# Kernel optimization log

Hardware: AMD Instinct MI355X
Metric: run time of the kernel (lower is better)

## Reference

```python
import jax, jax.numpy as jnp
import numpy as np

N_NODES = 100000
N_EDGES = 1600000
N_GRAPHS = 512
F_IN = 20
HID = 128
OUT = HID // 2


def _glorot(key, shape):
    fan_in, fan_out = shape[0], shape[1]
    lim = float(np.sqrt(6.0 / (fan_in + fan_out)))
    return jax.random.uniform(key, shape, jnp.float32, -lim, lim)


def setup_inputs() -> dict:
    key = jax.random.key(0)
    ks = jax.random.split(key, 12)
    x = jax.random.normal(ks[0], (N_NODES, F_IN), jnp.float32)
    edge_index = jax.random.randint(ks[1], (2, N_EDGES), 0, N_NODES, dtype=jnp.int64)
    batch = jnp.sort(jax.random.randint(ks[2], (N_NODES,), 0, N_GRAPHS, dtype=jnp.int64))
    return {
        "x": x,
        "edge_index": edge_index,
        "batch": batch,
        "W1": _glorot(ks[3], (F_IN, HID)), "b1": jnp.zeros((HID,), jnp.float32),
        "W2": _glorot(ks[4], (HID, HID)), "b2": jnp.zeros((HID,), jnp.float32),
        "W3": _glorot(ks[5], (HID, HID)), "b3": jnp.zeros((HID,), jnp.float32),
        "Wout": _glorot(ks[6], (HID, OUT)), "bout": jnp.zeros((OUT,), jnp.float32),
    }


def _gcn_conv(x, W, b, src, dst, num_nodes):
    # PyG GCNConv: x' = D^{-1/2} (A + I) D^{-1/2} X W + b (self-loops already in src/dst)
    xw = x @ W                                                  # [N, H]
    ones = jnp.ones(src.shape[0], dtype=xw.dtype)
    deg = jax.ops.segment_sum(ones, dst, num_segments=num_nodes)
    dinv = jnp.where(deg > 0, jax.lax.rsqrt(deg), 0.0)          # [N]
    norm = dinv[src] * dinv[dst]                                # [E+N]
    msg = xw[src] * norm[:, None]                               # gather + scale
    return jax.ops.segment_sum(msg, dst, num_segments=num_nodes) + b


def reference(x, edge_index, batch, W1, b1, W2, b2, W3, b3, Wout, bout):
    num_nodes = x.shape[0]
    loops = jnp.arange(num_nodes, dtype=edge_index.dtype)
    src = jnp.concatenate([edge_index[0], loops])
    dst = jnp.concatenate([edge_index[1], loops])

    h = jax.nn.relu(_gcn_conv(x, W1, b1, src, dst, num_nodes))
    h = jax.nn.relu(_gcn_conv(h, W2, b2, src, dst, num_nodes))
    h = jax.nn.relu(_gcn_conv(h, W3, b3, src, dst, num_nodes))

    # global_mean_pool over graph ids
    sums = jax.ops.segment_sum(h, batch, num_segments=N_GRAPHS)
    counts = jax.ops.segment_sum(jnp.ones(num_nodes, h.dtype), batch, num_segments=N_GRAPHS)
    pooled = sums / jnp.maximum(counts, 1.0)[:, None]           # [G, H]
    return pooled @ Wout + bout                                 # [G, H//2]
```

## Files before the change

kernel.cpp:

```cpp
#include <hip/hip_runtime.h>
#include <hip/hip_fp16.h>

#define N_NODES 100000
#define N_EDGES 1600000
#define N_GRAPHS 512
#define F_IN 20
#define HID 128
#define OUT_F 64

#define BUCKETS 256
#define SPAN 391
#define BCAP 7000
#define EPB 4096

typedef _Float16 half8_t __attribute__((ext_vector_type(8)));
typedef float f32x4_t __attribute__((ext_vector_type(4)));

__device__ inline float4 h4_to_f4(uint2 u) {
    __half2 h0 = *(__half2*)&u.x;
    __half2 h1 = *(__half2*)&u.y;
    float2 f0 = __half22float2(h0);
    float2 f1 = __half22float2(h1);
    return make_float4(f0.x, f0.y, f1.x, f1.y);
}

__global__ __launch_bounds__(512) void partition(const int* __restrict__ src,
                                                 const int* __restrict__ dst,
                                                 int* __restrict__ bpairs,
                                                 int* cur256) {
    __shared__ int lcnt[8][BUCKETS];
    __shared__ int woff[8][BUCKETS];
    int t = threadIdx.x;
    int wv = t >> 6;
    for (int i = t; i < 8 * BUCKETS; i += 512) ((int*)lcnt)[i] = 0;
    __syncthreads();
    int base = blockIdx.x * EPB;
    int myb[8], myp[8], myr[8];
#pragma unroll
    for (int i = 0; i < 8; ++i) {
        int e = base + i * 512 + t;
        int b = -1, p = 0, rk = 0;
        if (e < N_EDGES) {
            int s = src[e], d = dst[e];
            b = d / SPAN;
            p = (s << 9) | (d - b * SPAN);
            rk = atomicAdd(&lcnt[wv][b], 1);
        }
        myb[i] = b; myp[i] = p; myr[i] = rk;
    }
    __syncthreads();
    if (t < BUCKETS) {
        int c[8], tot = 0;
#pragma unroll
        for (int w = 0; w < 8; ++w) { c[w] = lcnt[w][t]; tot += c[w]; }
        int gb = atomicAdd(&cur256[t], tot);
#pragma unroll
        for (int w = 0; w < 8; ++w) { woff[w][t] = gb; gb += c[w]; }
    }
    __syncthreads();
#pragma unroll
    for (int i = 0; i < 8; ++i) {
        int b = myb[i];
        if (b >= 0) {
            int p = woff[wv][b] + myr[i];
            if (p < BCAP) bpairs[(size_t)b * BCAP + p] = myp[i];
        }
    }
}

__global__ __launch_bounds__(512) void csr_build(const int* __restrict__ bpairs,
                                                 const int* __restrict__ cur256,
                                                 int* __restrict__ row_st,
                                                 int* __restrict__ csr,
                                                 const float* __restrict__ x,
                                                 __half* __restrict__ Xs) {
    __shared__ int ocnt[SPAN];
    __shared__ int sc[512];
    __shared__ int cur[SPAN];
    __shared__ int sbase;
    int b = blockIdx.x, t = threadIdx.x;

    int myc = (t < BUCKETS) ? cur256[t] : 0;
    sc[t] = myc;
    __syncthreads();
    for (int o = 1; o < BUCKETS; o <<= 1) {
        int v = (t >= o) ? sc[t - o] : 0;
        __syncthreads();
        sc[t] += v;
        __syncthreads();
    }
    if (t == b) sbase = sc[t] - myc;
    if (b == BUCKETS - 1 && t == 0) row_st[N_NODES] = N_EDGES;

    int n0 = b * SPAN;
    int span = N_NODES - n0; if (span > SPAN) span = SPAN;
    if (t < SPAN) ocnt[t] = 0;
    __syncthreads();

    int n = cur256[b];
    const int* p = bpairs + (size_t)b * BCAP;
    for (int i = t; i < n; i += 512) atomicAdd(&ocnt[p[i] & 511], 1);
    __syncthreads();
    sc[t] = (t < span) ? ocnt[t] : 0;
    __syncthreads();
    for (int o = 1; o < 512; o <<= 1) {
        int v = (t >= o) ? sc[t - o] : 0;
        __syncthreads();
        sc[t] += v;
        __syncthreads();
    }
    int base = sbase;
    if (t < span) {
        int start = sc[t] - ocnt[t];
        row_st[n0 + t] = base + start;
        cur[t] = start;
    }
    __syncthreads();
    for (int i = t; i < n; i += 512) {
        int e = p[i];
        int lp = atomicAdd(&cur[e & 511], 1);
        csr[base + lp] = e >> 9;
    }
    for (int i = t; i < span * 32; i += 512) {
        int nl = i >> 5, f = i & 31;
        float v = (f < F_IN) ? x[(size_t)(n0 + nl) * F_IN + f] : 0.f;
        float di = rsqrtf((float)(ocnt[nl] + 1));
        Xs[(size_t)(n0 + nl) * 32 + f] = __float2half(di * v);
    }
}

__global__ __launch_bounds__(256) void layer1(const __half* __restrict__ Xs,
                                              const int* __restrict__ row_st,
                                              const int* __restrict__ csr,
                                              const float* __restrict__ W,
                                              const float* __restrict__ bias,
                                              __half* __restrict__ H) {
    __shared__ float Wlds[F_IN * HID];
    __shared__ float Alds[16 * F_IN];
    const int t = threadIdx.x;
    const int node0 = blockIdx.x * 16;

    for (int i = t; i < F_IN * HID; i += 256) Wlds[i] = W[i];

    const int h16 = t >> 4;
    const int l16 = t & 15;
    const __half2* X2 = (const __half2*)Xs;
    {
        int nn = node0 + h16;
        int r0 = row_st[nn], r1 = row_st[nn + 1];
        float2 f = __half22float2(X2[(size_t)nn * 16 + l16]);
        float2 acc = f;
        int r = r0;
        for (; r + 1 < r1; r += 2) {
            float2 f0 = __half22float2(X2[(size_t)csr[r] * 16 + l16]);
            float2 f1 = __half22float2(X2[(size_t)csr[r + 1] * 16 + l16]);
            acc.x += f0.x + f1.x;
            acc.y += f0.y + f1.y;
        }
        if (r < r1) {
            float2 f2 = __half22float2(X2[(size_t)csr[r] * 16 + l16]);
            acc.x += f2.x; acc.y += f2.y;
        }
        if (l16 < 10) {
            float di = rsqrtf((float)(r1 - r0 + 1));
            Alds[h16 * F_IN + l16 * 2]     = di * acc.x;
            Alds[h16 * F_IN + l16 * 2 + 1] = di * acc.y;
        }
    }
    __syncthreads();

    const int g  = t >> 5;
    const int h4 = (t & 31) * 4;
    float4 b4 = *(const float4*)&bias[h4];
    float4 acc0 = b4;
    float4 acc1 = b4;
#pragma unroll
    for (int kk = 0; kk < F_IN; ++kk) {
        float a0 = Alds[(g * 2) * F_IN + kk];
        float a1 = Alds[(g * 2 + 1) * F_IN + kk];
        float4 w = *(const float4*)&Wlds[kk * HID + h4];
        acc0.x = fmaf(a0, w.x, acc0.x);
        acc0.y = fmaf(a0, w.y, acc0.y);
        acc0.z = fmaf(a0, w.z, acc0.z);
        acc0.w = fmaf(a0, w.w, acc0.w);
        acc1.x = fmaf(a1, w.x, acc1.x);
        acc1.y = fmaf(a1, w.y, acc1.y);
        acc1.z = fmaf(a1, w.z, acc1.z);
        acc1.w = fmaf(a1, w.w, acc1.w);
    }
    {
        __half2 h0 = __floats2half2_rn(acc0.x, acc0.y);
        __half2 h1 = __floats2half2_rn(acc0.z, acc0.w);
        uint2 u; u.x = *(unsigned*)&h0; u.y = *(unsigned*)&h1;
        ((uint2*)H)[(node0 + g * 2) * 32 + (h4 >> 2)] = u;
    }
    {
        __half2 h0 = __floats2half2_rn(acc1.x, acc1.y);
        __half2 h1 = __floats2half2_rn(acc1.z, acc1.w);
        uint2 u; u.x = *(unsigned*)&h0; u.y = *(unsigned*)&h1;
        ((uint2*)H)[(node0 + g * 2 + 1) * 32 + (h4 >> 2)] = u;
    }
}

__global__ __launch_bounds__(256) void gemm_mfma(const __half* __restrict__ H,
                                                 const float* __restrict__ W,
                                                 const int* __restrict__ row_st,
                                                 __half* __restrict__ T) {
    __shared__ _Float16 Whi[64 * 128];
    __shared__ _Float16 Wlo[64 * 128];
    const int t = threadIdx.x;
    const int c0 = (blockIdx.x & 1) * 64;

    for (int i = t; i < 128 * 64; i += 256) {
        int k = i >> 6, c = i & 63;
        float w = W[k * HID + c0 + c];
        _Float16 hi = (_Float16)w;
        _Float16 lo = (_Float16)((w - (float)hi) * 2048.0f);
        int addr = c * 128 + (((k >> 3) ^ (c & 15)) << 3) + (k & 7);
        Whi[addr] = hi;
        Wlo[addr] = lo;
    }
    __syncthreads();

    const int wv = t >> 6;
    const int l  = t & 63;
    const int lr = l & 15;
    const int lq = l >> 4;

    for (int rep = 0; rep < 4; ++rep) {
        int strip = ((blockIdx.x >> 1) * 4 + wv) * 4 + rep;
        if (strip >= N_NODES / 16) continue;
        int n0 = strip * 16;

        f32x4_t acc[4], acl[4];
#pragma unroll
        for (int ct = 0; ct < 4; ++ct) { acc[ct] = (f32x4_t){0,0,0,0}; acl[ct] = (f32x4_t){0,0,0,0}; }

#pragma unroll
        for (int kc = 0; kc < 4; ++kc) {
            half8_t a = *(const half8_t*)(H + (size_t)(n0 + lr) * 128 + kc * 32 + lq * 8);
#pragma unroll
            for (int j = 0; j < 8; ++j) a[j] = a[j] > (_Float16)0 ? a[j] : (_Float16)0;
            int g = kc * 4 + lq;
#pragma unroll
            for (int ct = 0; ct < 4; ++ct) {
                int c = ct * 16 + lr;
                int addr = c * 128 + ((g ^ lr) << 3);
                half8_t bh = *(const half8_t*)&Whi[addr];
                half8_t bl = *(const half8_t*)&Wlo[addr];
                acc[ct] = __builtin_amdgcn_mfma_f32_16x16x32_f16(a, bh, acc[ct], 0, 0, 0);
                acl[ct] = __builtin_amdgcn_mfma_f32_16x16x32_f16(a, bl, acl[ct], 0, 0, 0);
            }
        }

        int r0 = n0 + lq * 4;
#pragma unroll
        for (int r = 0; r < 4; ++r) {
            int row = r0 + r;
            float d = rsqrtf((float)(row_st[row + 1] - row_st[row] + 1));
#pragma unroll
            for (int ct = 0; ct < 4; ++ct) {
                float v = (acc[ct][r] + acl[ct][r] * 4.8828125e-4f) * d;
                T[(size_t)row * 128 + c0 + ct * 16 + lr] = __float2half(v);
            }
        }
    }
}

__global__ __launch_bounds__(256) void gather_range(const __half* __restrict__ A,
                                                    const int* __restrict__ row_st,
                                                    const int* __restrict__ csr,
                                                    const float* __restrict__ bias,
                                                    __half* __restrict__ B) {
    int t = threadIdx.x;
    int n = blockIdx.x * 8 + (t >> 5);
    int l = t & 31;
    int r0 = row_st[n], r1 = row_st[n + 1];
    float di = rsqrtf((float)(r1 - r0 + 1));
    const uint2* Af = (const uint2*)A;
    float4 acc = h4_to_f4(Af[n * 32 + l]);
    int r = r0;
    for (; r + 7 < r1; r += 8) {
        int s0 = csr[r],     s1 = csr[r + 1], s2 = csr[r + 2], s3 = csr[r + 3];
        int s4 = csr[r + 4], s5 = csr[r + 5], s6 = csr[r + 6], s7 = csr[r + 7];
        float4 v0 = h4_to_f4(Af[s0 * 32 + l]);
        float4 v1 = h4_to_f4(Af[s1 * 32 + l]);
        float4 v2 = h4_to_f4(Af[s2 * 32 + l]);
        float4 v3 = h4_to_f4(Af[s3 * 32 + l]);
        float4 v4 = h4_to_f4(Af[s4 * 32 + l]);
        float4 v5 = h4_to_f4(Af[s5 * 32 + l]);
        float4 v6 = h4_to_f4(Af[s6 * 32 + l]);
        float4 v7 = h4_to_f4(Af[s7 * 32 + l]);
        acc.x += ((v0.x + v1.x) + (v2.x + v3.x)) + ((v4.x + v5.x) + (v6.x + v7.x));
        acc.y += ((v0.y + v1.y) + (v2.y + v3.y)) + ((v4.y + v5.y) + (v6.y + v7.y));
        acc.z += ((v0.z + v1.z) + (v2.z + v3.z)) + ((v4.z + v5.z) + (v6.z + v7.z));
        acc.w += ((v0.w + v1.w) + (v2.w + v3.w)) + ((v4.w + v5.w) + (v6.w + v7.w));
    }
    for (; r + 3 < r1; r += 4) {
        int s0 = csr[r], s1 = csr[r + 1], s2 = csr[r + 2], s3 = csr[r + 3];
        float4 v0 = h4_to_f4(Af[s0 * 32 + l]);
        float4 v1 = h4_to_f4(Af[s1 * 32 + l]);
        float4 v2 = h4_to_f4(Af[s2 * 32 + l]);
        float4 v3 = h4_to_f4(Af[s3 * 32 + l]);
        acc.x += (v0.x + v1.x) + (v2.x + v3.x);
        acc.y += (v0.y + v1.y) + (v2.y + v3.y);
        acc.z += (v0.z + v1.z) + (v2.z + v3.z);
        acc.w += (v0.w + v1.w) + (v2.w + v3.w);
    }
    for (; r < r1; ++r) {
        float4 v = h4_to_f4(Af[csr[r] * 32 + l]);
        acc.x += v.x; acc.y += v.y; acc.z += v.z; acc.w += v.w;
    }
    float4 b4 = ((const float4*)bias)[l];
    __half2 h0 = __floats2half2_rn(fmaf(di, acc.x, b4.x), fmaf(di, acc.y, b4.y));
    __half2 h1 = __floats2half2_rn(fmaf(di, acc.z, b4.z), fmaf(di, acc.w, b4.w));
    uint2 u; u.x = *(unsigned*)&h0; u.y = *(unsigned*)&h1;
    ((uint2*)B)[n * 32 + l] = u;
}

__global__ __launch_bounds__(256) void pool(const __half* __restrict__ B,
                                            const int* __restrict__ batch,
                                            float* sums, float* counts) {
    int t = threadIdx.x;
    int grp = blockIdx.x * 8 + (t >> 5);
    int l = t & 31;
    int h4 = l * 4;
    int n0 = grp * 8;
    if (n0 >= N_NODES) return;
    const uint2* Bf = (const uint2*)B;
    int cur = batch[n0];
    int runlen = 0;
    float4 acc = make_float4(0.f, 0.f, 0.f, 0.f);
    for (int k = 0; k < 8; ++k) {
        int n = n0 + k;
        if (n >= N_NODES) break;
        int g = batch[n];
        if (g != cur) {
            float* sp = &sums[cur * HID + h4];
            atomicAdd(sp + 0, acc.x); atomicAdd(sp + 1, acc.y);
            atomicAdd(sp + 2, acc.z); atomicAdd(sp + 3, acc.w);
            if (l == 0) atomicAdd(&counts[cur], (float)runlen);
            acc = make_float4(0.f, 0.f, 0.f, 0.f);
            runlen = 0;
            cur = g;
        }
        float4 v = h4_to_f4(Bf[n * 32 + l]);
        acc.x += fmaxf(v.x, 0.f);
        acc.y += fmaxf(v.y, 0.f);
        acc.z += fmaxf(v.z, 0.f);
        acc.w += fmaxf(v.w, 0.f);
        ++runlen;
    }
    float* sp = &sums[cur * HID + h4];
    atomicAdd(sp + 0, acc.x); atomicAdd(sp + 1, acc.y);
    atomicAdd(sp + 2, acc.z); atomicAdd(sp + 3, acc.w);
    if (l == 0) atomicAdd(&counts[cur], (float)runlen);
}

__global__ void final_gemm(const float* __restrict__ sums, const float* __restrict__ counts,
                           const float* __restrict__ Wout, const float* __restrict__ bout,
                           float* __restrict__ out) {
    int g = blockIdx.x;
    int o = threadIdx.x;
    __shared__ float p[HID];
    for (int k = o; k < HID; k += 64) p[k] = sums[g * HID + k];
    __syncthreads();
    float inv = 1.0f / fmaxf(counts[g], 1.0f);
    float acc = 0.f;
#pragma unroll 8
    for (int k = 0; k < HID; ++k)
        acc = fmaf(p[k], Wout[k * OUT_F + o], acc);
    out[g * OUT_F + o] = fmaf(inv, acc, bout[o]);
}

extern "C" void kernel_launch(void* const* d_in, const int* in_sizes, int n_in,
                              void* d_out, int out_size, void* d_ws, size_t ws_size,
                              hipStream_t stream) {
    const float* x     = (const float*)d_in[0];
    const int*   ei    = (const int*)d_in[1];
    const int*   batch = (const int*)d_in[2];
    const float* W1    = (const float*)d_in[3];
    const float* b1    = (const float*)d_in[4];
    const float* W2    = (const float*)d_in[5];
    const float* b2    = (const float*)d_in[6];
    const float* W3    = (const float*)d_in[7];
    const float* b3    = (const float*)d_in[8];
    const float* Wout  = (const float*)d_in[9];
    const float* bout  = (const float*)d_in[10];
    float* out = (float*)d_out;

    const int* src = ei;
    const int* dst = ei + N_EDGES;

    float* A      = (float*)d_ws;
    float* Breg   = A + (size_t)N_NODES * HID;
    int*   row_st = (int*)(Breg + (size_t)N_NODES * HID);
    float* sums   = (float*)(row_st + N_NODES + 1);
    float* counts = sums + N_GRAPHS * HID;
    int*   cur256 = (int*)(counts + N_GRAPHS);
    int*   csr    = cur256 + BUCKETS;

    int*    bpairs = (int*)A;
    __half* Xs     = (__half*)((char*)A + 7168000);
    __half* T      = (__half*)A;
    __half* H      = (__half*)Breg;

    hipMemsetAsync(sums, 0, (size_t)(N_GRAPHS * HID + N_GRAPHS + BUCKETS) * 4, stream);
    partition<<<(N_EDGES + EPB - 1) / EPB, 512, 0, stream>>>(src, dst, bpairs, cur256);
    csr_build<<<BUCKETS, 512, 0, stream>>>(bpairs, cur256, row_st, csr, x, Xs);

    layer1<<<N_NODES / 16, 256, 0, stream>>>(Xs, row_st, csr, W1, b1, H);

    gemm_mfma<<<782, 256, 0, stream>>>(H, W2, row_st, T);
    gather_range<<<N_NODES / 8, 256, 0, stream>>>(T, row_st, csr, b2, H);
    gemm_mfma<<<782, 256, 0, stream>>>(H, W3, row_st, T);
    gather_range<<<N_NODES / 8, 256, 0, stream>>>(T, row_st, csr, b3, H);

    pool<<<(N_NODES / 8 + 7) / 8, 256, 0, stream>>>(H, batch, sums, counts);
    final_gemm<<<N_GRAPHS, 64, 0, stream>>>(sums, counts, Wout, bout, out);
}
```

Measured before the change: 386.1 us.

## Fuse mean-pool with output GEMM per graph and double CSR partition buckets

Replaces the atomic-based pooling kernel and separate final GEMM with one kernel per graph that binary-searches the sorted batch array for its node range, reduces in shared memory, and applies Wout. This drops atomics, a kernel launch, and most of the memset. It also doubles the bucket count for CSR construction so each csr_build block handles a smaller span with more parallelism. The per-bucket capacity becomes tight relative to the average bucket load, and overflow is clamped rather than handled.

```diff
diff --git a/kernel.cpp b/kernel.cpp
--- a/kernel.cpp
+++ b/kernel.cpp
@@ -8,9 +8,9 @@
 #define HID 128
 #define OUT_F 64
 
-#define BUCKETS 256
-#define SPAN 391
-#define BCAP 7000
+#define BUCKETS 512
+#define SPAN 196
+#define BCAP 3500
 #define EPB 4096
 
 typedef _Float16 half8_t __attribute__((ext_vector_type(8)));
@@ -27,7 +27,7 @@
 __global__ __launch_bounds__(512) void partition(const int* __restrict__ src,
                                                  const int* __restrict__ dst,
                                                  int* __restrict__ bpairs,
-                                                 int* cur256) {
+                                                 int* cur512) {
     __shared__ int lcnt[8][BUCKETS];
     __shared__ int woff[8][BUCKETS];
     int t = threadIdx.x;
@@ -49,11 +49,11 @@
         myb[i] = b; myp[i] = p; myr[i] = rk;
     }
     __syncthreads();
-    if (t < BUCKETS) {
+    {
         int c[8], tot = 0;
 #pragma unroll
         for (int w = 0; w < 8; ++w) { c[w] = lcnt[w][t]; tot += c[w]; }
-        int gb = atomicAdd(&cur256[t], tot);
+        int gb = atomicAdd(&cur512[t], tot);
 #pragma unroll
         for (int w = 0; w < 8; ++w) { woff[w][t] = gb; gb += c[w]; }
     }
@@ -69,7 +69,7 @@
 }
 
 __global__ __launch_bounds__(512) void csr_build(const int* __restrict__ bpairs,
-                                                 const int* __restrict__ cur256,
+                                                 const int* __restrict__ cur512,
                                                  int* __restrict__ row_st,
                                                  int* __restrict__ csr,
                                                  const float* __restrict__ x,
@@ -80,7 +80,7 @@
     __shared__ int sbase;
     int b = blockIdx.x, t = threadIdx.x;
 
-    int myc = (t < BUCKETS) ? cur256[t] : 0;
+    int myc = cur512[t];
     sc[t] = myc;
     __syncthreads();
     for (int o = 1; o < BUCKETS; o <<= 1) {
@@ -94,10 +94,12 @@
 
     int n0 = b * SPAN;
     int span = N_NODES - n0; if (span > SPAN) span = SPAN;
+    if (span < 0) span = 0;
     if (t < SPAN) ocnt[t] = 0;
     __syncthreads();
 
-    int n = cur256[b];
+    int n = cur512[b];
+    if (n > BCAP) n = BCAP;
     const int* p = bpairs + (size_t)b * BCAP;
     for (int i = t; i < n; i += 512) atomicAdd(&ocnt[p[i] & 511], 1);
     __syncthreads();
@@ -318,59 +320,60 @@
     ((uint2*)B)[n * 32 + l] = u;
 }
 
-__global__ __launch_bounds__(256) void pool(const __half* __restrict__ B,
-                                            const int* __restrict__ batch,
-                                            float* sums, float* counts) {
+__global__ __launch_bounds__(256) void pool_head(const __half* __restrict__ H,
+                                                 const int* __restrict__ batch,
+                                                 const float* __restrict__ Wout,
+                                                 const float* __restrict__ bout,
+                                                 float* __restrict__ out) {
+    __shared__ float4 part[8][32];
+    __shared__ float p[HID];
+    __shared__ int bounds[2];
+    int g = blockIdx.x;
     int t = threadIdx.x;
-    int grp = blockIdx.x * 8 + (t >> 5);
-    int l = t & 31;
-    int h4 = l * 4;
-    int n0 = grp * 8;
-    if (n0 >= N_NODES) return;
-    const uint2* Bf = (const uint2*)B;
-    int cur = batch[n0];
-    int runlen = 0;
+    if (t < 2) {
+        int target = g + t;
+        int lo = 0, hi = N_NODES;
+        while (lo < hi) {
+            int mid = (lo + hi) >> 1;
+            if (batch[mid] < target) lo = mid + 1; else hi = mid;
+        }
+        bounds[t] = lo;
+    }
+    __syncthreads();
+    int lo = bounds[0], hi = bounds[1];
+    int grp = t >> 5, l = t & 31;
+    const uint2* Hf = (const uint2*)H;
     float4 acc = make_float4(0.f, 0.f, 0.f, 0.f);
-    for (int k = 0; k < 8; ++k) {
-        int n = n0 + k;
-        if (n >= N_NODES) break;
-        int g = batch[n];
-        if (g != cur) {
-            float* sp = &sums[cur * HID + h4];
-            atomicAdd(sp + 0, acc.x); atomicAdd(sp + 1, acc.y);
-            atomicAdd(sp + 2, acc.z); atomicAdd(sp + 3, acc.w);
-            if (l == 0) atomicAdd(&counts[cur], (float)runlen);
-            acc = make_float4(0.f, 0.f, 0.f, 0.f);
-            runlen = 0;
-            cur = g;
-        }
-        float4 v = h4_to_f4(Bf[n * 32 + l]);
+    for (int n = lo + grp; n < hi; n += 8) {
+        float4 v = h4_to_f4(Hf[(size_t)n * 32 + l]);
         acc.x += fmaxf(v.x, 0.f);
         acc.y += fmaxf(v.y, 0.f);
         acc.z += fmaxf(v.z, 0.f);
         acc.w += fmaxf(v.w, 0.f);
-        ++runlen;
-    }
-    float* sp = &sums[cur * HID + h4];
-    atomicAdd(sp + 0, acc.x); atomicAdd(sp + 1, acc.y);
-    atomicAdd(sp + 2, acc.z); atomicAdd(sp + 3, acc.w);
-    if (l == 0) atomicAdd(&counts[cur], (float)runlen);
-}
-
-__global__ void final_gemm(const float* __restrict__ sums, const float* __restrict__ counts,
-                           const float* __restrict__ Wout, const float* __restrict__ bout,
-                           float* __restrict__ out) {
-    int g = blockIdx.x;
-    int o = threadIdx.x;
-    __shared__ float p[HID];
-    for (int k = o; k < HID; k += 64) p[k] = sums[g * HID + k];
-    __syncthreads();
-    float inv = 1.0f / fmaxf(counts[g], 1.0f);
-    float acc = 0.f;
+    }
+    part[grp][l] = acc;
+    __syncthreads();
+    if (t < 32) {
+        float4 s = part[0][t];
+#pragma unroll
+        for (int j = 1; j < 8; ++j) {
+            float4 v = part[j][t];
+            s.x += v.x; s.y += v.y; s.z += v.z; s.w += v.w;
+        }
+        float inv = 1.0f / fmaxf((float)(hi - lo), 1.0f);
+        p[t * 4 + 0] = s.x * inv;
+        p[t * 4 + 1] = s.y * inv;
+        p[t * 4 + 2] = s.z * inv;
+        p[t * 4 + 3] = s.w * inv;
+    }
+    __syncthreads();
+    if (t < OUT_F) {
+        float acc2 = 0.f;
 #pragma unroll 8
-    for (int k = 0; k < HID; ++k)
-        acc = fmaf(p[k], Wout[k * OUT_F + o], acc);
-    out[g * OUT_F + o] = fmaf(inv, acc, bout[o]);
+        for (int k = 0; k < HID; ++k)
+            acc2 = fmaf(p[k], Wout[k * OUT_F + t], acc2);
+        out[g * OUT_F + t] = acc2 + bout[t];
+    }
 }
 
 extern "C" void kernel_launch(void* const* d_in, const int* in_sizes, int n_in,
@@ -395,19 +398,17 @@
     float* A      = (float*)d_ws;
     float* Breg   = A + (size_t)N_NODES * HID;
     int*   row_st = (int*)(Breg + (size_t)N_NODES * HID);
-    float* sums   = (float*)(row_st + N_NODES + 1);
-    float* counts = sums + N_GRAPHS * HID;
-    int*   cur256 = (int*)(counts + N_GRAPHS);
-    int*   csr    = cur256 + BUCKETS;
+    int*   cur512 = row_st + N_NODES + 1;
+    int*   csr    = cur512 + BUCKETS;
 
     int*    bpairs = (int*)A;
     __half* Xs     = (__half*)((char*)A + 7168000);
     __half* T      = (__half*)A;
     __half* H      = (__half*)Breg;
 
-    hipMemsetAsync(sums, 0, (size_t)(N_GRAPHS * HID + N_GRAPHS + BUCKETS) * 4, stream);
-    partition<<<(N_EDGES + EPB - 1) / EPB, 512, 0, stream>>>(src, dst, bpairs, cur256);
-    csr_build<<<BUCKETS, 512, 0, stream>>>(bpairs, cur256, row_st, csr, x, Xs);
+    hipMemsetAsync(cur512, 0, BUCKETS * sizeof(int), stream);
+    partition<<<(N_EDGES + EPB - 1) / EPB, 512, 0, stream>>>(src, dst, bpairs, cur512);
+    csr_build<<<BUCKETS, 512, 0, stream>>>(bpairs, cur512, row_st, csr, x, Xs);
 
     layer1<<<N_NODES / 16, 256, 0, stream>>>(Xs, row_st, csr, W1, b1, H);
 
@@ -416,6 +417,5 @@
     gemm_mfma<<<782, 256, 0, stream>>>(H, W3, row_st, T);
     gather_range<<<N_NODES / 8, 256, 0, stream>>>(T, row_st, csr, b3, H);
 
-    pool<<<(N_NODES / 8 + 7) / 8, 256, 0, stream>>>(H, batch, sums, counts);
-    final_gemm<<<N_GRAPHS, 64, 0, stream>>>(sums, counts, Wout, bout, out);
-}
+    pool_head<<<N_GRAPHS, 256, 0, stream>>>(H, batch, Wout, bout, out);
+}
```

Result: faster. 355.1 us (median of 2 runs) (-8.0%).
